# Performance work log

Measured on AMD Instinct MI355X. Metric: run time of the kernel, lower is better.

Reference implementation:

```python
import jax, jax.numpy as jnp
import numpy as np

B, L, HP, H, W = 4, 32, 32, 64, 64
D, DFFN, MAXL = 32, 64, 128

def setup_inputs() -> dict:
    key = jax.random.key(0)
    ks = jax.random.split(key, 20)
    rn = lambda k, s, sc=0.1: jax.random.normal(k, s, jnp.float32) * sc
    return {
        'x': jax.random.normal(ks[0], (B, 2 * L * HP, H, W), jnp.float32),
        'in_proj_w': rn(ks[1], (D, 12)), 'in_proj_b': rn(ks[2], (D,)),
        'layer_emb': rn(ks[3], (MAXL, D)),
        'time_decay': rn(ks[4], (D,)), 'time_first': rn(ks[5], (D,)),
        'ln_tm_g': jnp.ones((D,)), 'ln_tm_b': jnp.zeros((D,)),
        'tm_r': rn(ks[6], (D, D)), 'tm_k': rn(ks[7], (D, D)),
        'tm_v': rn(ks[8], (D, D)), 'tm_out': rn(ks[9], (D, D)),
        'ln_cm_g': jnp.ones((D,)), 'ln_cm_b': jnp.zeros((D,)),
        'cm_k': rn(ks[10], (DFFN, D)), 'cm_v': rn(ks[11], (D, DFFN)), 'cm_r': rn(ks[12], (D, D)),
        'gate_w': rn(ks[13], (1, D)), 'gate_b': rn(ks[14], (1,)),
        'row_w': rn(ks[15], (H, D)), 'row_b': rn(ks[16], (H,)),
        'col_w': rn(ks[17], (W, D)), 'col_b': rn(ks[18], (W,)),
    }

def _ln(x, g, b, eps=1e-5):
    mu = x.mean(-1, keepdims=True)
    var = ((x - mu) ** 2).mean(-1, keepdims=True)
    return (x - mu) * jax.lax.rsqrt(var + eps) * g + b

def _stats(a, b):
    # a, b: [B, L, HP, H, W] -> [B, L, HP, 12]
    af = a.reshape(*a.shape[:-2], -1)
    bf = b.reshape(*b.shape[:-2], -1)
    hs = lambda f: jnp.stack([f.mean(-1), f.std(-1, ddof=1), f.min(-1), f.max(-1)], -1)
    d = af - bf
    dm = d.mean(-1, keepdims=True)
    ds = d.std(-1, ddof=1, keepdims=True)
    dl2 = jnp.linalg.norm(d, axis=-1, keepdims=True)
    na = jnp.maximum(jnp.linalg.norm(af, axis=-1), 1e-8)
    nb = jnp.maximum(jnp.linalg.norm(bf, axis=-1), 1e-8)
    cos = ((af * bf).sum(-1) / (na * nb))[..., None]
    return jnp.concatenate([hs(af), hs(bf), dm, ds, dl2, cos], -1)

def reference(x, in_proj_w, in_proj_b, layer_emb, time_decay, time_first,
              ln_tm_g, ln_tm_b, tm_r, tm_k, tm_v, tm_out,
              ln_cm_g, ln_cm_b, cm_k, cm_v, cm_r,
              gate_w, gate_b, row_w, row_b, col_w, col_b):
    n = L * HP
    a = x[:, :n].reshape(B, L, HP, H, W)
    b = x[:, n:].reshape(B, L, HP, H, W)
    stats = _stats(a, b)                                   # [B,L,HP,12]
    feat_in = jnp.einsum('blhs,ds->blhd', stats, in_proj_w) + in_proj_b \
        + layer_emb[:L][None, :, None, :]
    feat_in = jnp.transpose(feat_in, (1, 0, 2, 3))         # [L,B,HP,D]
    wdec = jnp.exp(time_decay)

    def step(state, f):
        aa, bb, pp = state
        xn = _ln(f, ln_tm_g, ln_tm_b)
        r = jax.nn.sigmoid(xn @ tm_r.T)
        k = xn @ tm_k.T
        v = xn @ tm_v.T
        ww = time_first + k
        p = jnp.maximum(pp, ww)
        e1 = jnp.exp(pp - p)
        e2 = jnp.exp(ww - p)
        wkv = (e1 * aa + e2 * v) / jnp.maximum(e1 * bb + e2, 1e-8)
        ww2 = pp - wdec
        p2 = jnp.maximum(ww2, k)
        e1b = jnp.exp(ww2 - p2)
        e2b = jnp.exp(k - p2)
        y = f + r * (wkv @ tm_out.T)
        xn2 = _ln(y, ln_cm_g, ln_cm_b)
        kk = jnp.square(jax.nn.relu(xn2 @ cm_k.T))
        y = y + jax.nn.sigmoid(xn2 @ cm_r.T) * (kk @ cm_v.T)
        return (e1b * aa + e2b * v, e1b * bb + e2b, p2), y

    z = jnp.zeros((B, HP, D), x.dtype)
    init = (z, z, jnp.full((B, HP, D), -1e30, x.dtype))
    _, feats = jax.lax.scan(step, init, feat_in)           # [L,B,HP,D]

    gate = feats @ gate_w.T + gate_b                       # [L,B,HP,1]
    row = feats @ row_w.T + row_b                          # [L,B,HP,H]
    col = feats @ col_w.T + col_b                          # [L,B,HP,W]
    mask = jax.nn.sigmoid(gate[..., None] + row[..., None] + col[..., None, :])
    aT = jnp.transpose(a, (1, 0, 2, 3, 4))
    bT = jnp.transpose(b, (1, 0, 2, 3, 4))
    merged = mask * aT + (1.0 - mask) * bT                 # [L,B,HP,H,W]
    mixed = jnp.transpose(merged, (1, 0, 2, 3, 4)).reshape(B, n, H, W)
    return mixed, jax.nn.sigmoid(gate).mean(), mask.mean()
```

## Files before the change

### kernel.cpp

```cpp
#include <hip/hip_runtime.h>
#include <math.h>


__device__ __forceinline__ float sigf(float v) { return 1.0f / (1.0f + __expf(-v)); }

__global__ __launch_bounds__(256) void k_stats(
    const float* __restrict__ x, const float* __restrict__ in_proj_w,
    const float* __restrict__ in_proj_b, const float* __restrict__ layer_emb,
    const float* __restrict__ ln_tm_g, const float* __restrict__ ln_tm_b,
    const float* __restrict__ tm_r, const float* __restrict__ tm_k,
    const float* __restrict__ tm_v,
    float* __restrict__ f_out, float* __restrict__ r_out,
    float* __restrict__ k_out, float* __restrict__ v_out)
{
    __shared__ float red[4][9];
    __shared__ float tot[9];
    __shared__ __align__(16) float xn_s[32];
    const int bid = blockIdx.x;
    const int hp = bid & 31, l = (bid >> 5) & 31, bb = bid >> 10;
    const float4* pa = (const float4*)(x + (size_t)(bb * 2048 + l * 32 + hp) * 4096);
    const float4* pb = (const float4*)(x + (size_t)(bb * 2048 + 1024 + l * 32 + hp) * 4096);
    const int t = threadIdx.x;
    const int gidx = ((l * 4 + bb) * 32 + hp) * 32;

    float sa = 0.f, saa = 0.f, sb = 0.f, sbb = 0.f, sab = 0.f;
    float mna = 3.4e38f, mxa = -3.4e38f, mnb = 3.4e38f, mxb = -3.4e38f;
#pragma unroll
    for (int it = 0; it < 4; ++it) {
        float4 a4 = pa[t + it * 256];
        float4 b4 = pb[t + it * 256];
        sa  += a4.x + a4.y + a4.z + a4.w;
        sb  += b4.x + b4.y + b4.z + b4.w;
        saa += a4.x * a4.x + a4.y * a4.y + a4.z * a4.z + a4.w * a4.w;
        sbb += b4.x * b4.x + b4.y * b4.y + b4.z * b4.z + b4.w * b4.w;
        sab += a4.x * b4.x + a4.y * b4.y + a4.z * b4.z + a4.w * b4.w;
        mna = fminf(mna, fminf(fminf(a4.x, a4.y), fminf(a4.z, a4.w)));
        mxa = fmaxf(mxa, fmaxf(fmaxf(a4.x, a4.y), fmaxf(a4.z, a4.w)));
        mnb = fminf(mnb, fminf(fminf(b4.x, b4.y), fminf(b4.z, b4.w)));
        mxb = fmaxf(mxb, fmaxf(fmaxf(b4.x, b4.y), fmaxf(b4.z, b4.w)));
    }
#pragma unroll
    for (int m = 1; m < 64; m <<= 1) {
        sa  += __shfl_xor(sa, m);
        saa += __shfl_xor(saa, m);
        sb  += __shfl_xor(sb, m);
        sbb += __shfl_xor(sbb, m);
        sab += __shfl_xor(sab, m);
        mna = fminf(mna, __shfl_xor(mna, m));
        mxa = fmaxf(mxa, __shfl_xor(mxa, m));
        mnb = fminf(mnb, __shfl_xor(mnb, m));
        mxb = fmaxf(mxb, __shfl_xor(mxb, m));
    }
    const int lane = t & 63, wv = t >> 6;
    if (lane == 0) {
        red[wv][0] = sa;  red[wv][1] = saa; red[wv][2] = sb;  red[wv][3] = sbb;
        red[wv][4] = sab; red[wv][5] = mna; red[wv][6] = mxa; red[wv][7] = mnb;
        red[wv][8] = mxb;
    }
    __syncthreads();
    if (t == 0) {
#pragma unroll
        for (int q = 0; q < 5; ++q) tot[q] = red[0][q] + red[1][q] + red[2][q] + red[3][q];
        tot[5] = fminf(fminf(red[0][5], red[1][5]), fminf(red[2][5], red[3][5]));
        tot[6] = fmaxf(fmaxf(red[0][6], red[1][6]), fmaxf(red[2][6], red[3][6]));
        tot[7] = fminf(fminf(red[0][7], red[1][7]), fminf(red[2][7], red[3][7]));
        tot[8] = fmaxf(fmaxf(red[0][8], red[1][8]), fmaxf(red[2][8], red[3][8]));
    }
    __syncthreads();
    if (t < 32) {
        const float SA = tot[0], SAA = tot[1], SB = tot[2], SBB = tot[3], SAB = tot[4];
        const float inv_n = 1.f / 4096.f, inv_nm1 = 1.f / 4095.f;
        float st[12];
        st[0] = SA * inv_n;
        st[1] = sqrtf(fmaxf(SAA - SA * SA * inv_n, 0.f) * inv_nm1);
        st[2] = tot[5]; st[3] = tot[6];
        st[4] = SB * inv_n;
        st[5] = sqrtf(fmaxf(SBB - SB * SB * inv_n, 0.f) * inv_nm1);
        st[6] = tot[7]; st[7] = tot[8];
        const float SD = SA - SB, SDD = SAA - 2.f * SAB + SBB;
        st[8]  = SD * inv_n;
        st[9]  = sqrtf(fmaxf(SDD - SD * SD * inv_n, 0.f) * inv_nm1);
        st[10] = sqrtf(fmaxf(SDD, 0.f));
        const float na = fmaxf(sqrtf(SAA), 1e-8f), nb2 = fmaxf(sqrtf(SBB), 1e-8f);
        st[11] = SAB / (na * nb2);
        float fv = in_proj_b[t] + layer_emb[l * 32 + t];
#pragma unroll
        for (int s2 = 0; s2 < 12; ++s2) fv += st[s2] * in_proj_w[t * 12 + s2];
        f_out[gidx + t] = fv;
        float s = fv, q = fv * fv;
#pragma unroll
        for (int m = 1; m < 32; m <<= 1) { s += __shfl_xor(s, m, 32); q += __shfl_xor(q, m, 32); }
        const float mu = s * (1.f / 32.f);
        const float var = fmaxf(q * (1.f / 32.f) - mu * mu, 0.f);
        xn_s[t] = (fv - mu) * rsqrtf(var + 1e-5f) * ln_tm_g[t] + ln_tm_b[t];
    }
    __syncthreads();
    if (t < 96) {
        const int d = t & 31;
        const float* wrow = (t < 32 ? tm_r : (t < 64 ? tm_k : tm_v)) + d * 32;
        const float4* w4 = (const float4*)wrow;
        const float4* x4 = (const float4*)xn_s;
        float a0 = 0.f, a1 = 0.f, a2 = 0.f, a3 = 0.f;
#pragma unroll
        for (int jq = 0; jq < 2; ++jq) {
            float4 w, xv;
            w = w4[jq];     xv = x4[jq];     a0 += w.x*xv.x + w.y*xv.y + w.z*xv.z + w.w*xv.w;
            w = w4[jq + 2]; xv = x4[jq + 2]; a1 += w.x*xv.x + w.y*xv.y + w.z*xv.z + w.w*xv.w;
            w = w4[jq + 4]; xv = x4[jq + 4]; a2 += w.x*xv.x + w.y*xv.y + w.z*xv.z + w.w*xv.w;
            w = w4[jq + 6]; xv = x4[jq + 6]; a3 += w.x*xv.x + w.y*xv.y + w.z*xv.z + w.w*xv.w;
        }
        const float dot = (a0 + a1) + (a2 + a3);
        if (t < 32)      r_out[gidx + d] = sigf(dot);
        else if (t < 64) k_out[gidx + d] = dot;
        else             v_out[gidx + d] = dot;
    }
}

__global__ __launch_bounds__(256) void k_wkv(
    const float* __restrict__ k_in, const float* __restrict__ v_in,
    const float* __restrict__ time_decay, const float* __restrict__ time_first,
    float* __restrict__ wkv_out)
{
    const int ch = blockIdx.x * 256 + threadIdx.x;
    const int d = ch & 31;
    const float tf = time_first[d];
    const float wd = __expf(time_decay[d]);
    float aa = 0.f, bbs = 0.f, pp = -1e30f;
    float kc = k_in[ch], vc = v_in[ch];
#pragma unroll 4
    for (int l = 0; l < 32; ++l) {
        float kn = 0.f, vn = 0.f;
        if (l < 31) { kn = k_in[(l + 1) * 4096 + ch]; vn = v_in[(l + 1) * 4096 + ch]; }
        const float ww = tf + kc;
        const float p = fmaxf(pp, ww);
        const float e1 = __expf(pp - p), e2 = __expf(ww - p);
        wkv_out[l * 4096 + ch] = (e1 * aa + e2 * vc) / fmaxf(e1 * bbs + e2, 1e-8f);
        const float ww2 = pp - wd;
        const float p2 = fmaxf(ww2, kc);
        const float e1b = __expf(ww2 - p2), e2b = __expf(kc - p2);
        aa = e1b * aa + e2b * vc;
        bbs = e1b * bbs + e2b;
        pp = p2;
        kc = kn; vc = vn;
    }
}

__global__ __launch_bounds__(256) void k_merge(
    const float* __restrict__ x,
    const float* __restrict__ f_in, const float* __restrict__ r_in,
    const float* __restrict__ wkv_in,
    const float* __restrict__ tm_out,
    const float* __restrict__ ln_cm_g, const float* __restrict__ ln_cm_b,
    const float* __restrict__ cm_k, const float* __restrict__ cm_v,
    const float* __restrict__ cm_r,
    const float* __restrict__ gate_w, const float* __restrict__ gate_b,
    const float* __restrict__ row_w, const float* __restrict__ row_b,
    const float* __restrict__ col_w, const float* __restrict__ col_b,
    float* __restrict__ out, float* __restrict__ gpart, float* __restrict__ mpart)
{
    __shared__ __align__(16) float wkv_s[32];
    __shared__ __align__(16) float xn2_s[32];
    __shared__ __align__(16) float kk_s[64];
    __shared__ float cr_s[32];
    __shared__ float fs[32];
    __shared__ float row_s[64], col_s[64];
    __shared__ float gate_sh;
    __shared__ float red2[4];
    const int bid = blockIdx.x;
    const int hp = bid & 31, l = (bid >> 5) & 31, bb = bid >> 10;
    const int t = threadIdx.x;
    const int gidx = ((l * 4 + bb) * 32 + hp) * 32;

    if (t < 32) wkv_s[t] = wkv_in[gidx + t];
    __syncthreads();
    float yv = 0.f;
    if (t < 32) {
        const float fv = f_in[gidx + t];
        const float rv = r_in[gidx + t];
        const float4* w4 = (const float4*)(tm_out + t * 32);
        const float4* x4 = (const float4*)wkv_s;
        float a0 = 0.f, a1 = 0.f, a2 = 0.f, a3 = 0.f;
#pragma unroll
        for (int jq = 0; jq < 2; ++jq) {
            float4 w, xv;
            w = w4[jq];     xv = x4[jq];     a0 += w.x*xv.x + w.y*xv.y + w.z*xv.z + w.w*xv.w;
            w = w4[jq + 2]; xv = x4[jq + 2]; a1 += w.x*xv.x + w.y*xv.y + w.z*xv.z + w.w*xv.w;
            w = w4[jq + 4]; xv = x4[jq + 4]; a2 += w.x*xv.x + w.y*xv.y + w.z*xv.z + w.w*xv.w;
            w = w4[jq + 6]; xv = x4[jq + 6]; a3 += w.x*xv.x + w.y*xv.y + w.z*xv.z + w.w*xv.w;
        }
        yv = fv + rv * ((a0 + a1) + (a2 + a3));
        float s = yv, q = yv * yv;
#pragma unroll
        for (int m = 1; m < 32; m <<= 1) { s += __shfl_xor(s, m, 32); q += __shfl_xor(q, m, 32); }
        const float mu = s * (1.f / 32.f);
        const float var = fmaxf(q * (1.f / 32.f) - mu * mu, 0.f);
        xn2_s[t] = (yv - mu) * rsqrtf(var + 1e-5f) * ln_cm_g[t] + ln_cm_b[t];
    }
    __syncthreads();
    if (t < 64) {
        const float4* w4 = (const float4*)(cm_k + t * 32);
        const float4* x4 = (const float4*)xn2_s;
        float a0 = 0.f, a1 = 0.f, a2 = 0.f, a3 = 0.f;
#pragma unroll
        for (int jq = 0; jq < 2; ++jq) {
            float4 w, xv;
            w = w4[jq];     xv = x4[jq];     a0 += w.x*xv.x + w.y*xv.y + w.z*xv.z + w.w*xv.w;
            w = w4[jq + 2]; xv = x4[jq + 2]; a1 += w.x*xv.x + w.y*xv.y + w.z*xv.z + w.w*xv.w;
            w = w4[jq + 4]; xv = x4[jq + 4]; a2 += w.x*xv.x + w.y*xv.y + w.z*xv.z + w.w*xv.w;
            w = w4[jq + 6]; xv = x4[jq + 6]; a3 += w.x*xv.x + w.y*xv.y + w.z*xv.z + w.w*xv.w;
        }
        float kk = fmaxf((a0 + a1) + (a2 + a3), 0.f);
        kk_s[t] = kk * kk;
    } else if (t < 96) {
        const int d = t - 64;
        const float4* w4 = (const float4*)(cm_r + d * 32);
        const float4* x4 = (const float4*)xn2_s;
        float a0 = 0.f, a1 = 0.f, a2 = 0.f, a3 = 0.f;
#pragma unroll
        for (int jq = 0; jq < 2; ++jq) {
            float4 w, xv;
            w = w4[jq];     xv = x4[jq];     a0 += w.x*xv.x + w.y*xv.y + w.z*xv.z + w.w*xv.w;
            w = w4[jq + 2]; xv = x4[jq + 2]; a1 += w.x*xv.x + w.y*xv.y + w.z*xv.z + w.w*xv.w;
            w = w4[jq + 4]; xv = x4[jq + 4]; a2 += w.x*xv.x + w.y*xv.y + w.z*xv.z + w.w*xv.w;
            w = w4[jq + 6]; xv = x4[jq + 6]; a3 += w.x*xv.x + w.y*xv.y + w.z*xv.z + w.w*xv.w;
        }
        cr_s[d] = sigf((a0 + a1) + (a2 + a3));
    }
    __syncthreads();
    if (t < 32) {
        const float4* w4 = (const float4*)(cm_v + t * 64);
        const float4* x4 = (const float4*)kk_s;
        float a0 = 0.f, a1 = 0.f, a2 = 0.f, a3 = 0.f;
#pragma unroll
        for (int jq = 0; jq < 4; ++jq) {
            float4 w, xv;
            w = w4[jq];      xv = x4[jq];      a0 += w.x*xv.x + w.y*xv.y + w.z*xv.z + w.w*xv.w;
            w = w4[jq + 4];  xv = x4[jq + 4];  a1 += w.x*xv.x + w.y*xv.y + w.z*xv.z + w.w*xv.w;
            w = w4[jq + 8];  xv = x4[jq + 8];  a2 += w.x*xv.x + w.y*xv.y + w.z*xv.z + w.w*xv.w;
            w = w4[jq + 12]; xv = x4[jq + 12]; a3 += w.x*xv.x + w.y*xv.y + w.z*xv.z + w.w*xv.w;
        }
        fs[t] = yv + cr_s[t] * ((a0 + a1) + (a2 + a3));
    }
    __syncthreads();
    if (t < 64) {
        float a0 = row_b[t], a1 = 0.f, a2 = 0.f, a3 = 0.f;
#pragma unroll
        for (int d2 = 0; d2 < 8; ++d2) {
            a0 += fs[d2]      * row_w[t * 32 + d2];
            a1 += fs[d2 + 8]  * row_w[t * 32 + d2 + 8];
            a2 += fs[d2 + 16] * row_w[t * 32 + d2 + 16];
            a3 += fs[d2 + 24] * row_w[t * 32 + d2 + 24];
        }
        row_s[t] = (a0 + a1) + (a2 + a3);
    } else if (t < 128) {
        const int w = t - 64;
        float a0 = col_b[w], a1 = 0.f, a2 = 0.f, a3 = 0.f;
#pragma unroll
        for (int d2 = 0; d2 < 8; ++d2) {
            a0 += fs[d2]      * col_w[w * 32 + d2];
            a1 += fs[d2 + 8]  * col_w[w * 32 + d2 + 8];
            a2 += fs[d2 + 16] * col_w[w * 32 + d2 + 16];
            a3 += fs[d2 + 24] * col_w[w * 32 + d2 + 24];
        }
        col_s[w] = (a0 + a1) + (a2 + a3);
    } else if (t == 128) {
        float acc = gate_b[0];
#pragma unroll
        for (int d2 = 0; d2 < 32; ++d2) acc += fs[d2] * gate_w[d2];
        gate_sh = acc;
    }
    __syncthreads();
    const float gate = gate_sh;
    const float4* pa = (const float4*)(x + (size_t)(bb * 2048 + l * 32 + hp) * 4096);
    const float4* pb = (const float4*)(x + (size_t)(bb * 2048 + 1024 + l * 32 + hp) * 4096);
    float4* po = (float4*)(out + (size_t)(bb * 1024 + l * 32 + hp) * 4096);

    float msum = 0.f;
#pragma unroll
    for (int it = 0; it < 4; ++it) {
        const int i = t + it * 256;
        const float4 a4 = pa[i];
        const float4 b4 = pb[i];
        const int h = i >> 4, w0 = (i & 15) * 4;
        const float gr = gate + row_s[h];
        const float m0 = sigf(gr + col_s[w0 + 0]);
        const float m1 = sigf(gr + col_s[w0 + 1]);
        const float m2 = sigf(gr + col_s[w0 + 2]);
        const float m3 = sigf(gr + col_s[w0 + 3]);
        float4 o;
        o.x = b4.x + m0 * (a4.x - b4.x);
        o.y = b4.y + m1 * (a4.y - b4.y);
        o.z = b4.z + m2 * (a4.z - b4.z);
        o.w = b4.w + m3 * (a4.w - b4.w);
        po[i] = o;
        msum += m0 + m1 + m2 + m3;
    }
#pragma unroll
    for (int m = 1; m < 64; m <<= 1) msum += __shfl_xor(msum, m);
    if ((t & 63) == 0) red2[t >> 6] = msum;
    __syncthreads();
    if (t == 0) {
        mpart[bid] = red2[0] + red2[1] + red2[2] + red2[3];
        gpart[bid] = sigf(gate);
    }
}

__global__ __launch_bounds__(256) void k_final(
    const float* __restrict__ gpart, const float* __restrict__ mpart,
    float* __restrict__ out)
{
    __shared__ float rg[4], rm[4];
    const int t = threadIdx.x;
    float gs = 0.f, ms = 0.f;
    for (int i = t; i < 4096; i += 256) { gs += gpart[i]; ms += mpart[i]; }
#pragma unroll
    for (int m = 1; m < 64; m <<= 1) { gs += __shfl_xor(gs, m); ms += __shfl_xor(ms, m); }
    if ((t & 63) == 0) { rg[t >> 6] = gs; rm[t >> 6] = ms; }
    __syncthreads();
    if (t == 0) {
        out[16777216] = (rg[0] + rg[1] + rg[2] + rg[3]) * (1.f / 4096.f);
        out[16777217] = (rm[0] + rm[1] + rm[2] + rm[3]) * (1.f / 16777216.f);
    }
}

extern "C" void kernel_launch(void* const* d_in, const int* in_sizes, int n_in,
                              void* d_out, int out_size, void* d_ws, size_t ws_size,
                              hipStream_t stream) {
    const float* x          = (const float*)d_in[0];
    const float* in_proj_w  = (const float*)d_in[1];
    const float* in_proj_b  = (const float*)d_in[2];
    const float* layer_emb  = (const float*)d_in[3];
    const float* time_decay = (const float*)d_in[4];
    const float* time_first = (const float*)d_in[5];
    const float* ln_tm_g    = (const float*)d_in[6];
    const float* ln_tm_b    = (const float*)d_in[7];
    const float* tm_r       = (const float*)d_in[8];
    const float* tm_k       = (const float*)d_in[9];
    const float* tm_v       = (const float*)d_in[10];
    const float* tm_out     = (const float*)d_in[11];
    const float* ln_cm_g    = (const float*)d_in[12];
    const float* ln_cm_b    = (const float*)d_in[13];
    const float* cm_k       = (const float*)d_in[14];
    const float* cm_v       = (const float*)d_in[15];
    const float* cm_r       = (const float*)d_in[16];
    const float* gate_w     = (const float*)d_in[17];
    const float* gate_b     = (const float*)d_in[18];
    const float* row_w      = (const float*)d_in[19];
    const float* row_b      = (const float*)d_in[20];
    const float* col_w      = (const float*)d_in[21];
    const float* col_b      = (const float*)d_in[22];
    float* out = (float*)d_out;

    float* wsf   = (float*)d_ws;
    float* f_ws   = wsf;
    float* r_ws   = wsf + 131072;
    float* k_ws   = wsf + 262144;
    float* v_ws   = wsf + 393216;
    float* wkv_ws = wsf + 524288;
    float* gpart  = wsf + 655360;
    float* mpart  = wsf + 659456;

    k_stats<<<dim3(4096), dim3(256), 0, stream>>>(
        x, in_proj_w, in_proj_b, layer_emb, ln_tm_g, ln_tm_b,
        tm_r, tm_k, tm_v, f_ws, r_ws, k_ws, v_ws);
    k_wkv<<<dim3(16), dim3(256), 0, stream>>>(k_ws, v_ws, time_decay, time_first, wkv_ws);
    k_merge<<<dim3(4096), dim3(256), 0, stream>>>(
        x, f_ws, r_ws, wkv_ws, tm_out, ln_cm_g, ln_cm_b, cm_k, cm_v, cm_r,
        gate_w, gate_b, row_w, row_b, col_w, col_b, out, gpart, mpart);
    k_final<<<dim3(1), dim3(256), 0, stream>>>(gpart, mpart, out);
}
```

Measured before the change: 298.2 us.

## Fuse WKV scan into merge kernel and reduce means via atomics

Drops the separate 16-block WKV scan kernel. Each merge block now recomputes the recurrence for its own (b,hp) channels from step 0 up to its layer l, reading k and v interleaved as float2. The final reduction kernel is replaced by per-block atomicAdds into the two scalar outputs, which the stats kernel zeroes first. This removes two launches and the serial, low-occupancy scan, at the cost of redundant scan work (up to 32 steps per block) and atomic contention on two addresses.

```diff
diff --git a/kernel.cpp b/kernel.cpp
--- a/kernel.cpp
+++ b/kernel.cpp
@@ -11,7 +11,7 @@
     const float* __restrict__ tm_r, const float* __restrict__ tm_k,
     const float* __restrict__ tm_v,
     float* __restrict__ f_out, float* __restrict__ r_out,
-    float* __restrict__ k_out, float* __restrict__ v_out)
+    float* __restrict__ kv_out, float* __restrict__ out)
 {
     __shared__ float red[4][9];
     __shared__ float tot[9];
@@ -22,6 +22,8 @@
     const float4* pb = (const float4*)(x + (size_t)(bb * 2048 + 1024 + l * 32 + hp) * 4096);
     const int t = threadIdx.x;
     const int gidx = ((l * 4 + bb) * 32 + hp) * 32;
+
+    if (bid == 0 && t == 0) { out[16777216] = 0.f; out[16777217] = 0.f; }
 
     float sa = 0.f, saa = 0.f, sb = 0.f, sbb = 0.f, sab = 0.f;
     float mna = 3.4e38f, mxa = -3.4e38f, mnb = 3.4e38f, mxb = -3.4e38f;
@@ -111,44 +113,16 @@
         }
         const float dot = (a0 + a1) + (a2 + a3);
         if (t < 32)      r_out[gidx + d] = sigf(dot);
-        else if (t < 64) k_out[gidx + d] = dot;
-        else             v_out[gidx + d] = dot;
+        else if (t < 64) kv_out[2 * (gidx + d)] = dot;
+        else             kv_out[2 * (gidx + d) + 1] = dot;
     }
 }
 
-__global__ __launch_bounds__(256) void k_wkv(
-    const float* __restrict__ k_in, const float* __restrict__ v_in,
-    const float* __restrict__ time_decay, const float* __restrict__ time_first,
-    float* __restrict__ wkv_out)
-{
-    const int ch = blockIdx.x * 256 + threadIdx.x;
-    const int d = ch & 31;
-    const float tf = time_first[d];
-    const float wd = __expf(time_decay[d]);
-    float aa = 0.f, bbs = 0.f, pp = -1e30f;
-    float kc = k_in[ch], vc = v_in[ch];
-#pragma unroll 4
-    for (int l = 0; l < 32; ++l) {
-        float kn = 0.f, vn = 0.f;
-        if (l < 31) { kn = k_in[(l + 1) * 4096 + ch]; vn = v_in[(l + 1) * 4096 + ch]; }
-        const float ww = tf + kc;
-        const float p = fmaxf(pp, ww);
-        const float e1 = __expf(pp - p), e2 = __expf(ww - p);
-        wkv_out[l * 4096 + ch] = (e1 * aa + e2 * vc) / fmaxf(e1 * bbs + e2, 1e-8f);
-        const float ww2 = pp - wd;
-        const float p2 = fmaxf(ww2, kc);
-        const float e1b = __expf(ww2 - p2), e2b = __expf(kc - p2);
-        aa = e1b * aa + e2b * vc;
-        bbs = e1b * bbs + e2b;
-        pp = p2;
-        kc = kn; vc = vn;
-    }
-}
-
-__global__ __launch_bounds__(256) void k_merge(
+__global__ __launch_bounds__(256) void k_fused(
     const float* __restrict__ x,
     const float* __restrict__ f_in, const float* __restrict__ r_in,
-    const float* __restrict__ wkv_in,
+    const float* __restrict__ kv_in,
+    const float* __restrict__ time_decay, const float* __restrict__ time_first,
     const float* __restrict__ tm_out,
     const float* __restrict__ ln_cm_g, const float* __restrict__ ln_cm_b,
     const float* __restrict__ cm_k, const float* __restrict__ cm_v,
@@ -156,7 +130,7 @@
     const float* __restrict__ gate_w, const float* __restrict__ gate_b,
     const float* __restrict__ row_w, const float* __restrict__ row_b,
     const float* __restrict__ col_w, const float* __restrict__ col_b,
-    float* __restrict__ out, float* __restrict__ gpart, float* __restrict__ mpart)
+    float* __restrict__ out)
 {
     __shared__ __align__(16) float wkv_s[32];
     __shared__ __align__(16) float xn2_s[32];
@@ -169,11 +143,36 @@
     const int bid = blockIdx.x;
     const int hp = bid & 31, l = (bid >> 5) & 31, bb = bid >> 10;
     const int t = threadIdx.x;
-    const int gidx = ((l * 4 + bb) * 32 + hp) * 32;
-
-    if (t < 32) wkv_s[t] = wkv_in[gidx + t];
-    __syncthreads();
+    const int chb = bb * 1024 + hp * 32;
+    const int gidx = l * 4096 + chb;
+
     float yv = 0.f;
+    if (t < 32) {
+        const float2* kv2p = (const float2*)kv_in;
+        const float tf = time_first[t];
+        const float wd = __expf(time_decay[t]);
+        float aa = 0.f, bbs = 0.f, pp = -1e30f;
+        float wkv = 0.f;
+#pragma unroll
+        for (int l2 = 0; l2 < 32; ++l2) {
+            const float2 kv2 = kv2p[l2 * 4096 + chb + t];
+            if (l2 < l) {
+                const float ww2 = pp - wd;
+                const float p2 = fmaxf(ww2, kv2.x);
+                const float e1b = __expf(ww2 - p2), e2b = __expf(kv2.x - p2);
+                aa = e1b * aa + e2b * kv2.y;
+                bbs = e1b * bbs + e2b;
+                pp = p2;
+            } else if (l2 == l) {
+                const float ww = tf + kv2.x;
+                const float p = fmaxf(pp, ww);
+                const float e1 = __expf(pp - p), e2 = __expf(ww - p);
+                wkv = (e1 * aa + e2 * kv2.y) / fmaxf(e1 * bbs + e2, 1e-8f);
+            }
+        }
+        wkv_s[t] = wkv;
+    }
+    __syncthreads();
     if (t < 32) {
         const float fv = f_in[gidx + t];
         const float rv = r_in[gidx + t];
@@ -300,26 +299,8 @@
     if ((t & 63) == 0) red2[t >> 6] = msum;
     __syncthreads();
     if (t == 0) {
-        mpart[bid] = red2[0] + red2[1] + red2[2] + red2[3];
-        gpart[bid] = sigf(gate);
-    }
-}
-
-__global__ __launch_bounds__(256) void k_final(
-    const float* __restrict__ gpart, const float* __restrict__ mpart,
-    float* __restrict__ out)
-{
-    __shared__ float rg[4], rm[4];
-    const int t = threadIdx.x;
-    float gs = 0.f, ms = 0.f;
-    for (int i = t; i < 4096; i += 256) { gs += gpart[i]; ms += mpart[i]; }
-#pragma unroll
-    for (int m = 1; m < 64; m <<= 1) { gs += __shfl_xor(gs, m); ms += __shfl_xor(ms, m); }
-    if ((t & 63) == 0) { rg[t >> 6] = gs; rm[t >> 6] = ms; }
-    __syncthreads();
-    if (t == 0) {
-        out[16777216] = (rg[0] + rg[1] + rg[2] + rg[3]) * (1.f / 4096.f);
-        out[16777217] = (rm[0] + rm[1] + rm[2] + rm[3]) * (1.f / 16777216.f);
+        atomicAdd(out + 16777217, (red2[0] + red2[1] + red2[2] + red2[3]) * (1.f / 16777216.f));
+        atomicAdd(out + 16777216, sigf(gate) * (1.f / 4096.f));
     }
 }
 
@@ -352,20 +333,15 @@
     float* out = (float*)d_out;
 
     float* wsf   = (float*)d_ws;
-    float* f_ws   = wsf;
-    float* r_ws   = wsf + 131072;
-    float* k_ws   = wsf + 262144;
-    float* v_ws   = wsf + 393216;
-    float* wkv_ws = wsf + 524288;
-    float* gpart  = wsf + 655360;
-    float* mpart  = wsf + 659456;
+    float* f_ws  = wsf;
+    float* r_ws  = wsf + 131072;
+    float* kv_ws = wsf + 262144;
 
     k_stats<<<dim3(4096), dim3(256), 0, stream>>>(
         x, in_proj_w, in_proj_b, layer_emb, ln_tm_g, ln_tm_b,
-        tm_r, tm_k, tm_v, f_ws, r_ws, k_ws, v_ws);
-    k_wkv<<<dim3(16), dim3(256), 0, stream>>>(k_ws, v_ws, time_decay, time_first, wkv_ws);
-    k_merge<<<dim3(4096), dim3(256), 0, stream>>>(
-        x, f_ws, r_ws, wkv_ws, tm_out, ln_cm_g, ln_cm_b, cm_k, cm_v, cm_r,
-        gate_w, gate_b, row_w, row_b, col_w, col_b, out, gpart, mpart);
-    k_final<<<dim3(1), dim3(256), 0, stream>>>(gpart, mpart, out);
+        tm_r, tm_k, tm_v, f_ws, r_ws, kv_ws, out);
+    k_fused<<<dim3(4096), dim3(256), 0, stream>>>(
+        x, f_ws, r_ws, kv_ws, time_decay, time_first, tm_out,
+        ln_cm_g, ln_cm_b, cm_k, cm_v, cm_r,
+        gate_w, gate_b, row_w, row_b, col_w, col_b, out);
 }
```

Measured after the change: 373.5 us. 1.25x slower.

## Prefetch merge inputs early, collapse merge MLP into one wave, replace final reduction with atomics

Applied to the files above, without the earlier changes.

The merge kernel now loads its a/b tiles into registers before the small per-token MLP. It runs that MLP inside a single 64-thread wave, using wave-level shuffles instead of block barriers, so the global load latency overlaps the compute and only one __syncthreads remains before the blend. The final reduction kernel is removed: the scalar means are accumulated with atomicAdd, and the stats kernel zeroes them first. The WKV scan now reads interleaved k/v as float2, preloads all 32 steps into registers, and spreads its work over 64 smaller blocks. The trade-offs are higher register pressure, ordering-dependent atomic float sums, and reliance on stream order for the zero-initialisation.

```diff
diff --git a/kernel.cpp b/kernel.cpp
--- a/kernel.cpp
+++ b/kernel.cpp
@@ -11,7 +11,7 @@
     const float* __restrict__ tm_r, const float* __restrict__ tm_k,
     const float* __restrict__ tm_v,
     float* __restrict__ f_out, float* __restrict__ r_out,
-    float* __restrict__ k_out, float* __restrict__ v_out)
+    float* __restrict__ kv_out, float* __restrict__ out)
 {
     __shared__ float red[4][9];
     __shared__ float tot[9];
@@ -22,6 +22,8 @@
     const float4* pb = (const float4*)(x + (size_t)(bb * 2048 + 1024 + l * 32 + hp) * 4096);
     const int t = threadIdx.x;
     const int gidx = ((l * 4 + bb) * 32 + hp) * 32;
+
+    if (bid == 0 && t == 0) { out[16777216] = 0.f; out[16777217] = 0.f; }
 
     float sa = 0.f, saa = 0.f, sb = 0.f, sbb = 0.f, sab = 0.f;
     float mna = 3.4e38f, mxa = -3.4e38f, mnb = 3.4e38f, mxb = -3.4e38f;
@@ -111,26 +113,28 @@
         }
         const float dot = (a0 + a1) + (a2 + a3);
         if (t < 32)      r_out[gidx + d] = sigf(dot);
-        else if (t < 64) k_out[gidx + d] = dot;
-        else             v_out[gidx + d] = dot;
+        else if (t < 64) kv_out[2 * (gidx + d)] = dot;
+        else             kv_out[2 * (gidx + d) + 1] = dot;
     }
 }
 
-__global__ __launch_bounds__(256) void k_wkv(
-    const float* __restrict__ k_in, const float* __restrict__ v_in,
+__global__ __launch_bounds__(64) void k_wkv(
+    const float* __restrict__ kv_in,
     const float* __restrict__ time_decay, const float* __restrict__ time_first,
     float* __restrict__ wkv_out)
 {
-    const int ch = blockIdx.x * 256 + threadIdx.x;
+    const int ch = blockIdx.x * 64 + threadIdx.x;
     const int d = ch & 31;
     const float tf = time_first[d];
     const float wd = __expf(time_decay[d]);
+    const float2* kv2 = (const float2*)kv_in;
+    float2 kv[32];
+#pragma unroll
+    for (int l = 0; l < 32; ++l) kv[l] = kv2[l * 4096 + ch];
     float aa = 0.f, bbs = 0.f, pp = -1e30f;
-    float kc = k_in[ch], vc = v_in[ch];
-#pragma unroll 4
+#pragma unroll
     for (int l = 0; l < 32; ++l) {
-        float kn = 0.f, vn = 0.f;
-        if (l < 31) { kn = k_in[(l + 1) * 4096 + ch]; vn = v_in[(l + 1) * 4096 + ch]; }
+        const float kc = kv[l].x, vc = kv[l].y;
         const float ww = tf + kc;
         const float p = fmaxf(pp, ww);
         const float e1 = __expf(pp - p), e2 = __expf(ww - p);
@@ -141,7 +145,6 @@
         aa = e1b * aa + e2b * vc;
         bbs = e1b * bbs + e2b;
         pp = p2;
-        kc = kn; vc = vn;
     }
 }
 
@@ -156,13 +159,12 @@
     const float* __restrict__ gate_w, const float* __restrict__ gate_b,
     const float* __restrict__ row_w, const float* __restrict__ row_b,
     const float* __restrict__ col_w, const float* __restrict__ col_b,
-    float* __restrict__ out, float* __restrict__ gpart, float* __restrict__ mpart)
+    float* __restrict__ out)
 {
     __shared__ __align__(16) float wkv_s[32];
     __shared__ __align__(16) float xn2_s[32];
     __shared__ __align__(16) float kk_s[64];
-    __shared__ float cr_s[32];
-    __shared__ float fs[32];
+    __shared__ __align__(16) float fs[32];
     __shared__ float row_s[64], col_s[64];
     __shared__ float gate_sh;
     __shared__ float red2[4];
@@ -171,116 +173,121 @@
     const int t = threadIdx.x;
     const int gidx = ((l * 4 + bb) * 32 + hp) * 32;
 
-    if (t < 32) wkv_s[t] = wkv_in[gidx + t];
-    __syncthreads();
-    float yv = 0.f;
-    if (t < 32) {
-        const float fv = f_in[gidx + t];
-        const float rv = r_in[gidx + t];
-        const float4* w4 = (const float4*)(tm_out + t * 32);
-        const float4* x4 = (const float4*)wkv_s;
-        float a0 = 0.f, a1 = 0.f, a2 = 0.f, a3 = 0.f;
-#pragma unroll
-        for (int jq = 0; jq < 2; ++jq) {
-            float4 w, xv;
-            w = w4[jq];     xv = x4[jq];     a0 += w.x*xv.x + w.y*xv.y + w.z*xv.z + w.w*xv.w;
-            w = w4[jq + 2]; xv = x4[jq + 2]; a1 += w.x*xv.x + w.y*xv.y + w.z*xv.z + w.w*xv.w;
-            w = w4[jq + 4]; xv = x4[jq + 4]; a2 += w.x*xv.x + w.y*xv.y + w.z*xv.z + w.w*xv.w;
-            w = w4[jq + 6]; xv = x4[jq + 6]; a3 += w.x*xv.x + w.y*xv.y + w.z*xv.z + w.w*xv.w;
-        }
-        yv = fv + rv * ((a0 + a1) + (a2 + a3));
-        float s = yv, q = yv * yv;
-#pragma unroll
-        for (int m = 1; m < 32; m <<= 1) { s += __shfl_xor(s, m, 32); q += __shfl_xor(q, m, 32); }
-        const float mu = s * (1.f / 32.f);
-        const float var = fmaxf(q * (1.f / 32.f) - mu * mu, 0.f);
-        xn2_s[t] = (yv - mu) * rsqrtf(var + 1e-5f) * ln_cm_g[t] + ln_cm_b[t];
-    }
-    __syncthreads();
-    if (t < 64) {
-        const float4* w4 = (const float4*)(cm_k + t * 32);
-        const float4* x4 = (const float4*)xn2_s;
-        float a0 = 0.f, a1 = 0.f, a2 = 0.f, a3 = 0.f;
-#pragma unroll
-        for (int jq = 0; jq < 2; ++jq) {
-            float4 w, xv;
-            w = w4[jq];     xv = x4[jq];     a0 += w.x*xv.x + w.y*xv.y + w.z*xv.z + w.w*xv.w;
-            w = w4[jq + 2]; xv = x4[jq + 2]; a1 += w.x*xv.x + w.y*xv.y + w.z*xv.z + w.w*xv.w;
-            w = w4[jq + 4]; xv = x4[jq + 4]; a2 += w.x*xv.x + w.y*xv.y + w.z*xv.z + w.w*xv.w;
-            w = w4[jq + 6]; xv = x4[jq + 6]; a3 += w.x*xv.x + w.y*xv.y + w.z*xv.z + w.w*xv.w;
-        }
-        float kk = fmaxf((a0 + a1) + (a2 + a3), 0.f);
-        kk_s[t] = kk * kk;
-    } else if (t < 96) {
-        const int d = t - 64;
-        const float4* w4 = (const float4*)(cm_r + d * 32);
-        const float4* x4 = (const float4*)xn2_s;
-        float a0 = 0.f, a1 = 0.f, a2 = 0.f, a3 = 0.f;
-#pragma unroll
-        for (int jq = 0; jq < 2; ++jq) {
-            float4 w, xv;
-            w = w4[jq];     xv = x4[jq];     a0 += w.x*xv.x + w.y*xv.y + w.z*xv.z + w.w*xv.w;
-            w = w4[jq + 2]; xv = x4[jq + 2]; a1 += w.x*xv.x + w.y*xv.y + w.z*xv.z + w.w*xv.w;
-            w = w4[jq + 4]; xv = x4[jq + 4]; a2 += w.x*xv.x + w.y*xv.y + w.z*xv.z + w.w*xv.w;
-            w = w4[jq + 6]; xv = x4[jq + 6]; a3 += w.x*xv.x + w.y*xv.y + w.z*xv.z + w.w*xv.w;
-        }
-        cr_s[d] = sigf((a0 + a1) + (a2 + a3));
-    }
-    __syncthreads();
-    if (t < 32) {
-        const float4* w4 = (const float4*)(cm_v + t * 64);
-        const float4* x4 = (const float4*)kk_s;
-        float a0 = 0.f, a1 = 0.f, a2 = 0.f, a3 = 0.f;
-#pragma unroll
-        for (int jq = 0; jq < 4; ++jq) {
-            float4 w, xv;
-            w = w4[jq];      xv = x4[jq];      a0 += w.x*xv.x + w.y*xv.y + w.z*xv.z + w.w*xv.w;
-            w = w4[jq + 4];  xv = x4[jq + 4];  a1 += w.x*xv.x + w.y*xv.y + w.z*xv.z + w.w*xv.w;
-            w = w4[jq + 8];  xv = x4[jq + 8];  a2 += w.x*xv.x + w.y*xv.y + w.z*xv.z + w.w*xv.w;
-            w = w4[jq + 12]; xv = x4[jq + 12]; a3 += w.x*xv.x + w.y*xv.y + w.z*xv.z + w.w*xv.w;
-        }
-        fs[t] = yv + cr_s[t] * ((a0 + a1) + (a2 + a3));
-    }
-    __syncthreads();
-    if (t < 64) {
-        float a0 = row_b[t], a1 = 0.f, a2 = 0.f, a3 = 0.f;
-#pragma unroll
-        for (int d2 = 0; d2 < 8; ++d2) {
-            a0 += fs[d2]      * row_w[t * 32 + d2];
-            a1 += fs[d2 + 8]  * row_w[t * 32 + d2 + 8];
-            a2 += fs[d2 + 16] * row_w[t * 32 + d2 + 16];
-            a3 += fs[d2 + 24] * row_w[t * 32 + d2 + 24];
-        }
-        row_s[t] = (a0 + a1) + (a2 + a3);
-    } else if (t < 128) {
-        const int w = t - 64;
-        float a0 = col_b[w], a1 = 0.f, a2 = 0.f, a3 = 0.f;
-#pragma unroll
-        for (int d2 = 0; d2 < 8; ++d2) {
-            a0 += fs[d2]      * col_w[w * 32 + d2];
-            a1 += fs[d2 + 8]  * col_w[w * 32 + d2 + 8];
-            a2 += fs[d2 + 16] * col_w[w * 32 + d2 + 16];
-            a3 += fs[d2 + 24] * col_w[w * 32 + d2 + 24];
-        }
-        col_s[w] = (a0 + a1) + (a2 + a3);
-    } else if (t == 128) {
-        float acc = gate_b[0];
-#pragma unroll
-        for (int d2 = 0; d2 < 32; ++d2) acc += fs[d2] * gate_w[d2];
-        gate_sh = acc;
-    }
-    __syncthreads();
-    const float gate = gate_sh;
     const float4* pa = (const float4*)(x + (size_t)(bb * 2048 + l * 32 + hp) * 4096);
     const float4* pb = (const float4*)(x + (size_t)(bb * 2048 + 1024 + l * 32 + hp) * 4096);
     float4* po = (float4*)(out + (size_t)(bb * 1024 + l * 32 + hp) * 4096);
 
+    float4 av[4], bv[4];
+#pragma unroll
+    for (int it = 0; it < 4; ++it) {
+        av[it] = pa[t + it * 256];
+        bv[it] = pb[t + it * 256];
+    }
+
+    if (t < 64) {
+        float yv = 0.f, y2 = 0.f;
+        if (t < 32) {
+            wkv_s[t] = wkv_in[gidx + t];
+            const float fv = f_in[gidx + t];
+            const float rv = r_in[gidx + t];
+            const float4* w4 = (const float4*)(tm_out + t * 32);
+            const float4* x4 = (const float4*)wkv_s;
+            float a0 = 0.f, a1 = 0.f, a2 = 0.f, a3 = 0.f;
+#pragma unroll
+            for (int jq = 0; jq < 2; ++jq) {
+                float4 w, xv;
+                w = w4[jq];     xv = x4[jq];     a0 += w.x*xv.x + w.y*xv.y + w.z*xv.z + w.w*xv.w;
+                w = w4[jq + 2]; xv = x4[jq + 2]; a1 += w.x*xv.x + w.y*xv.y + w.z*xv.z + w.w*xv.w;
+                w = w4[jq + 4]; xv = x4[jq + 4]; a2 += w.x*xv.x + w.y*xv.y + w.z*xv.z + w.w*xv.w;
+                w = w4[jq + 6]; xv = x4[jq + 6]; a3 += w.x*xv.x + w.y*xv.y + w.z*xv.z + w.w*xv.w;
+            }
+            yv = fv + rv * ((a0 + a1) + (a2 + a3));
+            float s = yv, q = yv * yv;
+#pragma unroll
+            for (int m = 1; m < 32; m <<= 1) { s += __shfl_xor(s, m, 32); q += __shfl_xor(q, m, 32); }
+            const float mu = s * (1.f / 32.f);
+            const float var = fmaxf(q * (1.f / 32.f) - mu * mu, 0.f);
+            xn2_s[t] = (yv - mu) * rsqrtf(var + 1e-5f) * ln_cm_g[t] + ln_cm_b[t];
+        }
+        {
+            const float4* w4 = (const float4*)(cm_k + t * 32);
+            const float4* x4 = (const float4*)xn2_s;
+            float a0 = 0.f, a1 = 0.f, a2 = 0.f, a3 = 0.f;
+#pragma unroll
+            for (int jq = 0; jq < 2; ++jq) {
+                float4 w, xv;
+                w = w4[jq];     xv = x4[jq];     a0 += w.x*xv.x + w.y*xv.y + w.z*xv.z + w.w*xv.w;
+                w = w4[jq + 2]; xv = x4[jq + 2]; a1 += w.x*xv.x + w.y*xv.y + w.z*xv.z + w.w*xv.w;
+                w = w4[jq + 4]; xv = x4[jq + 4]; a2 += w.x*xv.x + w.y*xv.y + w.z*xv.z + w.w*xv.w;
+                w = w4[jq + 6]; xv = x4[jq + 6]; a3 += w.x*xv.x + w.y*xv.y + w.z*xv.z + w.w*xv.w;
+            }
+            float kk = fmaxf((a0 + a1) + (a2 + a3), 0.f);
+            kk_s[t] = kk * kk;
+        }
+        if (t < 32) {
+            float cr;
+            {
+                const float4* w4 = (const float4*)(cm_r + t * 32);
+                const float4* x4 = (const float4*)xn2_s;
+                float a0 = 0.f, a1 = 0.f, a2 = 0.f, a3 = 0.f;
+#pragma unroll
+                for (int jq = 0; jq < 2; ++jq) {
+                    float4 w, xv;
+                    w = w4[jq];     xv = x4[jq];     a0 += w.x*xv.x + w.y*xv.y + w.z*xv.z + w.w*xv.w;
+                    w = w4[jq + 2]; xv = x4[jq + 2]; a1 += w.x*xv.x + w.y*xv.y + w.z*xv.z + w.w*xv.w;
+                    w = w4[jq + 4]; xv = x4[jq + 4]; a2 += w.x*xv.x + w.y*xv.y + w.z*xv.z + w.w*xv.w;
+                    w = w4[jq + 6]; xv = x4[jq + 6]; a3 += w.x*xv.x + w.y*xv.y + w.z*xv.z + w.w*xv.w;
+                }
+                cr = sigf((a0 + a1) + (a2 + a3));
+            }
+            {
+                const float4* w4 = (const float4*)(cm_v + t * 64);
+                const float4* x4 = (const float4*)kk_s;
+                float a0 = 0.f, a1 = 0.f, a2 = 0.f, a3 = 0.f;
+#pragma unroll
+                for (int jq = 0; jq < 4; ++jq) {
+                    float4 w, xv;
+                    w = w4[jq];      xv = x4[jq];      a0 += w.x*xv.x + w.y*xv.y + w.z*xv.z + w.w*xv.w;
+                    w = w4[jq + 4];  xv = x4[jq + 4];  a1 += w.x*xv.x + w.y*xv.y + w.z*xv.z + w.w*xv.w;
+                    w = w4[jq + 8];  xv = x4[jq + 8];  a2 += w.x*xv.x + w.y*xv.y + w.z*xv.z + w.w*xv.w;
+                    w = w4[jq + 12]; xv = x4[jq + 12]; a3 += w.x*xv.x + w.y*xv.y + w.z*xv.z + w.w*xv.w;
+                }
+                y2 = yv + cr * ((a0 + a1) + (a2 + a3));
+            }
+            fs[t] = y2;
+            float g = y2 * gate_w[t];
+#pragma unroll
+            for (int m = 1; m < 32; m <<= 1) g += __shfl_xor(g, m, 32);
+            if (t == 0) gate_sh = g + gate_b[0];
+        }
+        {
+            float a0 = row_b[t], a1 = 0.f, a2 = 0.f, a3 = 0.f;
+            float c0 = col_b[t], c1 = 0.f, c2 = 0.f, c3 = 0.f;
+#pragma unroll
+            for (int d2 = 0; d2 < 8; ++d2) {
+                const float f0 = fs[d2], f1 = fs[d2 + 8], f2 = fs[d2 + 16], f3 = fs[d2 + 24];
+                a0 += f0 * row_w[t * 32 + d2];
+                a1 += f1 * row_w[t * 32 + d2 + 8];
+                a2 += f2 * row_w[t * 32 + d2 + 16];
+                a3 += f3 * row_w[t * 32 + d2 + 24];
+                c0 += f0 * col_w[t * 32 + d2];
+                c1 += f1 * col_w[t * 32 + d2 + 8];
+                c2 += f2 * col_w[t * 32 + d2 + 16];
+                c3 += f3 * col_w[t * 32 + d2 + 24];
+            }
+            row_s[t] = (a0 + a1) + (a2 + a3);
+            col_s[t] = (c0 + c1) + (c2 + c3);
+        }
+    }
+    __syncthreads();
+
+    const float gate = gate_sh;
     float msum = 0.f;
 #pragma unroll
     for (int it = 0; it < 4; ++it) {
         const int i = t + it * 256;
-        const float4 a4 = pa[i];
-        const float4 b4 = pb[i];
+        const float4 a4 = av[it];
+        const float4 b4 = bv[it];
         const int h = i >> 4, w0 = (i & 15) * 4;
         const float gr = gate + row_s[h];
         const float m0 = sigf(gr + col_s[w0 + 0]);
@@ -300,26 +307,8 @@
     if ((t & 63) == 0) red2[t >> 6] = msum;
     __syncthreads();
     if (t == 0) {
-        mpart[bid] = red2[0] + red2[1] + red2[2] + red2[3];
-        gpart[bid] = sigf(gate);
-    }
-}
-
-__global__ __launch_bounds__(256) void k_final(
-    const float* __restrict__ gpart, const float* __restrict__ mpart,
-    float* __restrict__ out)
-{
-    __shared__ float rg[4], rm[4];
-    const int t = threadIdx.x;
-    float gs = 0.f, ms = 0.f;
-    for (int i = t; i < 4096; i += 256) { gs += gpart[i]; ms += mpart[i]; }
-#pragma unroll
-    for (int m = 1; m < 64; m <<= 1) { gs += __shfl_xor(gs, m); ms += __shfl_xor(ms, m); }
-    if ((t & 63) == 0) { rg[t >> 6] = gs; rm[t >> 6] = ms; }
-    __syncthreads();
-    if (t == 0) {
-        out[16777216] = (rg[0] + rg[1] + rg[2] + rg[3]) * (1.f / 4096.f);
-        out[16777217] = (rm[0] + rm[1] + rm[2] + rm[3]) * (1.f / 16777216.f);
+        atomicAdd(out + 16777217, (red2[0] + red2[1] + red2[2] + red2[3]) * (1.f / 16777216.f));
+        atomicAdd(out + 16777216, sigf(gate) * (1.f / 4096.f));
     }
 }
 
@@ -351,21 +340,18 @@
     const float* col_b      = (const float*)d_in[22];
     float* out = (float*)d_out;
 
-    float* wsf   = (float*)d_ws;
+    float* wsf    = (float*)d_ws;
     float* f_ws   = wsf;
     float* r_ws   = wsf + 131072;
-    float* k_ws   = wsf + 262144;
-    float* v_ws   = wsf + 393216;
+    float* kv_ws  = wsf + 262144;
     float* wkv_ws = wsf + 524288;
-    float* gpart  = wsf + 655360;
-    float* mpart  = wsf + 659456;
 
     k_stats<<<dim3(4096), dim3(256), 0, stream>>>(
         x, in_proj_w, in_proj_b, layer_emb, ln_tm_g, ln_tm_b,
-        tm_r, tm_k, tm_v, f_ws, r_ws, k_ws, v_ws);
-    k_wkv<<<dim3(16), dim3(256), 0, stream>>>(k_ws, v_ws, time_decay, time_first, wkv_ws);
+        tm_r, tm_k, tm_v, f_ws, r_ws, kv_ws, out);
+    k_wkv<<<dim3(64), dim3(64), 0, stream>>>(
+        kv_ws, time_decay, time_first, wkv_ws);
     k_merge<<<dim3(4096), dim3(256), 0, stream>>>(
         x, f_ws, r_ws, wkv_ws, tm_out, ln_cm_g, ln_cm_b, cm_k, cm_v, cm_r,
-        gate_w, gate_b, row_w, row_b, col_w, col_b, out, gpart, mpart);
-    k_final<<<dim3(1), dim3(256), 0, stream>>>(gpart, mpart, out);
+        gate_w, gate_b, row_w, row_b, col_w, col_b, out);
 }
```

Result: slower. 379.6 us (+27.3%).
